# Kernel tuning notes

Measured on AMD Instinct MI355X. Metric: run time of the kernel, lower is better.

## Reference

```python
import jax, jax.numpy as jnp
import numpy as np

N_HEADS = 16
HID_DIM = 64
INPUT_DIM = 1024
B, L = 4, 1024
NEG = -10000000000.0


def setup_inputs() -> dict:
    key = jax.random.key(0)
    ks = jax.random.split(key, 10)
    d = INPUT_DIM
    h = N_HEADS * HID_DIM
    s = 1.0 / np.sqrt(d)
    return {
        "query": jax.random.normal(ks[0], (B, L, d), dtype=jnp.float32),
        "key": jax.random.normal(ks[1], (B, L, d), dtype=jnp.float32),
        "value": jax.random.normal(ks[2], (B, L, d), dtype=jnp.float32),
        "mask": jax.random.randint(ks[3], (B, 1, L, L), 0, 2, dtype=jnp.int32),
        "wq": jax.random.normal(ks[4], (d, h), dtype=jnp.float32) * s,
        "bq": jnp.zeros((h,), dtype=jnp.float32),
        "wk": jax.random.normal(ks[5], (d, h), dtype=jnp.float32) * s,
        "bk": jnp.zeros((h,), dtype=jnp.float32),
        "wv": jax.random.normal(ks[6], (d, h), dtype=jnp.float32) * s,
        "bv": jnp.zeros((h,), dtype=jnp.float32),
    }


def _split_heads(x):
    # [B, L, H*D] -> [B, H, L, D]
    b, l, _ = x.shape
    return x.reshape(b, l, N_HEADS, HID_DIM).transpose(0, 2, 1, 3)


def reference(query, key, value, mask, wq, bq, wk, bk, wv, bv):
    scale = jnp.sqrt(jnp.float32(HID_DIM))
    Q = _split_heads(query @ wq + bq)   # [B,H,L,D]
    K = _split_heads(key @ wk + bk)
    V = _split_heads(value @ wv + bv)
    energy = jnp.einsum("bhqd,bhkd->bhqk", Q, K) / scale
    energy = jnp.where(mask == 0, jnp.float32(NEG), energy)
    attention = energy  # NOTE: softmax is intentionally skipped, as in the source
    x = jnp.einsum("bhqk,bhkd->bhqd", attention, V)
    x = x.transpose(0, 2, 1, 3).reshape(query.shape[0], -1, N_HEADS * HID_DIM)
    return (attention, x)
```

## Files before the change

### kernel.cpp

```cpp
#include <hip/hip_runtime.h>
#include <stdint.h>
#include <stddef.h>


typedef __attribute__((ext_vector_type(8))) short short8;
typedef __attribute__((ext_vector_type(4))) float f32x4;
typedef __attribute__((ext_vector_type(4))) int i32x4;
typedef __attribute__((ext_vector_type(2))) unsigned int u32x2;

#define MFMA16(a, b, c) __builtin_amdgcn_mfma_f32_16x16x32_bf16(a, b, c, 0, 0, 0)

using gptr_t = const __attribute__((address_space(1))) void*;
using lptr_t = __attribute__((address_space(3))) void*;

#define NEGV -10000000000.0f

__device__ __forceinline__ unsigned short f2bf(float f) {
  uint32_t u = __builtin_bit_cast(uint32_t, f);
  u += 0x7FFFu + ((u >> 16) & 1u);
  return (unsigned short)(u >> 16);
}

__global__ __launch_bounds__(256) void k_maskpack(const int* __restrict__ mask,
                                                  unsigned long long* __restrict__ mb) {
  const int wid = (blockIdx.x * 256 + threadIdx.x) >> 6;
  const int l = threadIdx.x & 63;
#pragma unroll 4
  for (int i = 0; i < 32; ++i) {
    const size_t c = (size_t)wid * 32 + i;
    const int v = mask[c * 64 + l];
    const unsigned long long bits = __ballot(v != 0);
    if (l == 0) mb[c] = bits;
  }
}

__global__ __launch_bounds__(256) void k_wt(
    const float* __restrict__ wq, const float* __restrict__ wk, const float* __restrict__ wv,
    unsigned short* __restrict__ tq, unsigned short* __restrict__ tk,
    unsigned short* __restrict__ tv) {
  const int z = blockIdx.z;
  const float* src = z == 0 ? wq : z == 1 ? wk : wv;
  unsigned short* dst = z == 0 ? tq : z == 1 ? tk : tv;
  __shared__ unsigned short t[64][65];
  const int n0 = blockIdx.x * 64, k0 = blockIdx.y * 64;
#pragma unroll
  for (int i = 0; i < 16; ++i) {
    const int idx = i * 256 + threadIdx.x;
    const int r = idx >> 6, c = idx & 63;
    t[r][c] = f2bf(src[(size_t)(k0 + r) * 1024 + n0 + c]);
  }
  __syncthreads();
#pragma unroll
  for (int i = 0; i < 16; ++i) {
    const int idx = i * 256 + threadIdx.x;
    const int r = idx >> 6, c = idx & 63;
    dst[(size_t)(n0 + r) * 1024 + k0 + c] = t[c][r];
  }
}

__global__ __launch_bounds__(256) void k_gemm(
    const float* __restrict__ Xq, const float* __restrict__ Xk,
    const float* __restrict__ Xv,
    const unsigned short* __restrict__ Wq, const unsigned short* __restrict__ Wk,
    const unsigned short* __restrict__ Wv,
    const float* __restrict__ bq, const float* __restrict__ bk, const float* __restrict__ bv,
    unsigned short* __restrict__ Cq, unsigned short* __restrict__ Ck,
    unsigned short* __restrict__ Vt) {
  const int z = blockIdx.z;
  const float* X           = z == 0 ? Xq : z == 1 ? Xk : Xv;
  const unsigned short* Wt = z == 0 ? Wq : z == 1 ? Wk : Wv;
  const float* bias        = z == 0 ? bq : z == 1 ? bk : bv;

  __shared__ unsigned short Ads[128 * 64];
  __shared__ unsigned short Bds[128 * 64];

  const int tid = threadIdx.x;
  const int w = tid >> 6, l = tid & 63;
  const int lr = l & 15, g = l >> 4;
  const int m0 = blockIdx.y * 128, n0 = blockIdx.x * 128;
  const int wm = (w >> 1) * 64, wn = (w & 1) * 64;
  const int srow = tid >> 3, sslot = tid & 7;

  f32x4 acc[4][4];
#pragma unroll
  for (int mi = 0; mi < 4; ++mi)
#pragma unroll
    for (int ni = 0; ni < 4; ++ni) acc[mi][ni] = (f32x4){0.f, 0.f, 0.f, 0.f};

  for (int kt = 0; kt < 16; ++kt) {
    const int kb = kt * 64;
#pragma unroll
    for (int i = 0; i < 4; ++i) {
      const int idx = i * 256 + tid;
      const int row = idx >> 3, c8 = idx & 7;
      const float* ga = X + (size_t)(m0 + row) * 1024 + kb + c8 * 8;
      f32x4 a0 = *(const f32x4*)ga;
      f32x4 a1 = *(const f32x4*)(ga + 4);
      short8 pk;
      pk[0] = (short)f2bf(a0[0]); pk[1] = (short)f2bf(a0[1]);
      pk[2] = (short)f2bf(a0[2]); pk[3] = (short)f2bf(a0[3]);
      pk[4] = (short)f2bf(a1[0]); pk[5] = (short)f2bf(a1[1]);
      pk[6] = (short)f2bf(a1[2]); pk[7] = (short)f2bf(a1[3]);
      *(short8*)&Ads[row * 64 + ((c8 ^ (row & 7)) << 3)] = pk;
    }
#pragma unroll
    for (int i = 0; i < 4; ++i) {
      const int row = i * 32 + srow;
      const int scol = ((sslot ^ (row & 7)) << 3);
      const unsigned short* gb = Wt + (size_t)(n0 + row) * 1024 + kb + scol;
      __builtin_amdgcn_global_load_lds((gptr_t)gb, (lptr_t)&Bds[(i * 32 + w * 8) * 64], 16, 0, 0);
    }
    __syncthreads();
    short8 afr[4][2], bfr[4][2];
#pragma unroll
    for (int t = 0; t < 4; ++t)
#pragma unroll
      for (int ks = 0; ks < 2; ++ks) {
        const int ra = wm + t * 16 + lr;
        afr[t][ks] = *(const short8*)&Ads[ra * 64 + (((ks * 4 + g) ^ (ra & 7)) << 3)];
        const int rb = wn + t * 16 + lr;
        bfr[t][ks] = *(const short8*)&Bds[rb * 64 + (((ks * 4 + g) ^ (rb & 7)) << 3)];
      }
#pragma unroll
    for (int ks = 0; ks < 2; ++ks)
#pragma unroll
      for (int mi = 0; mi < 4; ++mi)
#pragma unroll
        for (int ni = 0; ni < 4; ++ni)
          acc[mi][ni] = MFMA16(afr[mi][ks], bfr[ni][ks], acc[mi][ni]);
    __syncthreads();
  }

  if (z != 2) {
    unsigned short* C = z == 0 ? Cq : Ck;
#pragma unroll
    for (int mi = 0; mi < 4; ++mi)
#pragma unroll
      for (int ni = 0; ni < 4; ++ni) {
        const int n = n0 + wn + ni * 16 + lr;
        const float bs = bias[n];
        f32x4 a = acc[mi][ni];
#pragma unroll
        for (int r = 0; r < 4; ++r) {
          const int m = m0 + wm + mi * 16 + g * 4 + r;
          C[(size_t)m * 1024 + n] = f2bf(a[r] + bs);
        }
      }
  } else {
#pragma unroll
    for (int mi = 0; mi < 4; ++mi)
#pragma unroll
      for (int ni = 0; ni < 4; ++ni) {
        const int ng = n0 + wn + ni * 16 + lr;
        const int hh = ng >> 6, dd = ng & 63;
        const float bs = bias[ng];
        f32x4 a = acc[mi][ni];
        const int mg = m0 + wm + mi * 16 + g * 4;
        const int bb = mg >> 10;
        const int ll = mg & 1023;
        u32x2 pk;
        pk[0] = (uint32_t)f2bf(a[0] + bs) | ((uint32_t)f2bf(a[1] + bs) << 16);
        pk[1] = (uint32_t)f2bf(a[2] + bs) | ((uint32_t)f2bf(a[3] + bs) << 16);
        *(u32x2*)&Vt[(size_t)((bb * 16 + hh) * 64 + dd) * 1024 + ll] = pk;
      }
  }
}

__global__ __launch_bounds__(512, 4) void k_attn(
    const unsigned short* __restrict__ Qb, const unsigned short* __restrict__ Kb,
    const unsigned short* __restrict__ Vt, const uint32_t* __restrict__ mb,
    float* __restrict__ att, float* __restrict__ xout) {
  const int bh = blockIdx.y, b = bh >> 4, h = bh & 15;
  const int tid = threadIdx.x;
  const int w = tid >> 6, l = tid & 63;
  const int lr = l & 15, g = l >> 4;
  const int q0 = blockIdx.x * 128 + w * 16;

  __shared__ unsigned short Kl[128 * 64];
  __shared__ unsigned short Vl[64 * 128];
  __shared__ unsigned short Pl[8 * 16 * 128];
  unsigned short* Pw = &Pl[w * 16 * 128];

  short8 qf[2];
#pragma unroll
  for (int ks = 0; ks < 2; ++ks)
    qf[ks] = *(const short8*)&Qb[(size_t)(b * 1024 + q0 + lr) * 1024 +
                                 h * 64 + ks * 32 + g * 8];

  f32x4 xacc[4];
#pragma unroll
  for (int di = 0; di < 4; ++di) xacc[di] = (f32x4){0.f, 0.f, 0.f, 0.f};

  for (int kt = 0; kt < 8; ++kt) {
    const int kb = kt * 128;
    __syncthreads();
#pragma unroll
    for (int i = 0; i < 2; ++i) {
      const int row = i * 64 + (tid >> 3);
      const int slot = tid & 7;
      const unsigned short* src = Kb + (size_t)(b * 1024 + kb + row) * 1024 +
                                  h * 64 + ((slot ^ (row & 7)) << 3);
      __builtin_amdgcn_global_load_lds((gptr_t)src, (lptr_t)&Kl[(i * 64 + w * 8) * 64], 16, 0, 0);
    }
#pragma unroll
    for (int i = 0; i < 2; ++i) {
      const int row = i * 32 + (tid >> 4);
      const int slot = tid & 15;
      const unsigned short* src = Vt + (size_t)(bh * 64 + row) * 1024 + kb +
                                  ((slot ^ (row & 7)) << 3);
      __builtin_amdgcn_global_load_lds((gptr_t)src, (lptr_t)&Vl[(i * 32 + w * 4) * 128], 16, 0, 0);
    }
    const i32x4 mw = *(const i32x4*)&mb[(size_t)(b * 1024 + q0 + lr) * 32 + kt * 4];
    __syncthreads();

    f32x4 s[8];
#pragma unroll
    for (int ni = 0; ni < 8; ++ni) {
      f32x4 a = (f32x4){0.f, 0.f, 0.f, 0.f};
#pragma unroll
      for (int ks = 0; ks < 2; ++ks) {
        const int row = ni * 16 + lr;
        short8 kf = *(const short8*)&Kl[row * 64 + (((ks * 4 + g) ^ (row & 7)) << 3)];
        a = MFMA16(kf, qf[ks], a);
      }
      s[ni] = a;
    }
#pragma unroll
    for (int ni = 0; ni < 8; ++ni) {
      const uint32_t wbits = (uint32_t)mw[ni >> 1];
      const int bit0 = (ni & 1) * 16 + g * 4;
      f32x4 e;
#pragma unroll
      for (int j = 0; j < 4; ++j)
        e[j] = ((wbits >> (bit0 + j)) & 1u) ? s[ni][j] * 0.125f : NEGV;
      u32x2 pk;
      pk[0] = (uint32_t)f2bf(e[0]) | ((uint32_t)f2bf(e[1]) << 16);
      pk[1] = (uint32_t)f2bf(e[2]) | ((uint32_t)f2bf(e[3]) << 16);
      const int colq = ni * 16 + g * 4;
      *(u32x2*)&Pw[lr * 128 + (colq ^ ((lr & 7) << 3))] = pk;
    }
    asm volatile("s_waitcnt lgkmcnt(0)" ::: "memory");
    __builtin_amdgcn_sched_barrier(0);
#pragma unroll
    for (int p = 0; p < 8; ++p) {
      const int flat = p * 256 + l * 4;
      const int row = flat >> 7;
      const int col = flat & 127;
      u32x2 pr = *(const u32x2*)&Pw[row * 128 + (col ^ ((row & 7) << 3))];
      const uint32_t u0 = pr[0], u1 = pr[1];
      f32x4 e;
      e[0] = __builtin_bit_cast(float, u0 << 16);
      e[1] = __builtin_bit_cast(float, u0 & 0xFFFF0000u);
      e[2] = __builtin_bit_cast(float, u1 << 16);
      e[3] = __builtin_bit_cast(float, u1 & 0xFFFF0000u);
      __builtin_nontemporal_store(
          e, (f32x4*)&att[(size_t)(bh * 1024 + q0 + row) * 1024 + kb + col]);
    }
#pragma unroll
    for (int ks4 = 0; ks4 < 4; ++ks4) {
      const int colk = ks4 * 32 + g * 8;
      short8 pa = *(const short8*)&Pw[lr * 128 + (colk ^ ((lr & 7) << 3))];
#pragma unroll
      for (int di = 0; di < 4; ++di) {
        const int vr = di * 16 + lr;
        short8 vf = *(const short8*)&Vl[vr * 128 + (colk ^ ((vr & 7) << 3))];
        xacc[di] = MFMA16(pa, vf, xacc[di]);
      }
    }
    asm volatile("" ::: "memory");
  }

#pragma unroll
  for (int di = 0; di < 4; ++di) {
    f32x4 a = xacc[di];
#pragma unroll
    for (int r = 0; r < 4; ++r) {
      const int q = q0 + g * 4 + r;
      __builtin_nontemporal_store(
          a[r], &xout[(size_t)(b * 1024 + q) * 1024 + h * 64 + di * 16 + lr]);
    }
  }
}

extern "C" void kernel_launch(void* const* d_in, const int* in_sizes, int n_in,
                              void* d_out, int out_size, void* d_ws, size_t ws_size,
                              hipStream_t stream) {
  (void)in_sizes; (void)n_in; (void)out_size;
  const float* q   = (const float*)d_in[0];
  const float* k   = (const float*)d_in[1];
  const float* v   = (const float*)d_in[2];
  const int* mask  = (const int*)d_in[3];
  const float* wq  = (const float*)d_in[4];
  const float* bq  = (const float*)d_in[5];
  const float* wk  = (const float*)d_in[6];
  const float* bk  = (const float*)d_in[7];
  const float* wv  = (const float*)d_in[8];
  const float* bv  = (const float*)d_in[9];
  float* att = (float*)d_out;
  float* x   = att + (size_t)4 * 16 * 1024 * 1024;

  char* ws = (char*)d_ws;
  const size_t SZX = (size_t)4096 * 1024 * 2;
  const size_t SZW = (size_t)1024 * 1024 * 2;
  const size_t SZM = (size_t)4 * 1024 * 32 * 4;
  if (ws_size < 3 * SZX + 3 * SZW + SZM) return;
  unsigned short* Wtq = (unsigned short*)(ws);
  unsigned short* Wtk = (unsigned short*)(ws + SZW);
  unsigned short* Wtv = (unsigned short*)(ws + 2 * SZW);
  unsigned short* Qb  = (unsigned short*)(ws + 3 * SZW);
  unsigned short* Kb  = (unsigned short*)(ws + 3 * SZW + SZX);
  unsigned short* Vt  = (unsigned short*)(ws + 3 * SZW + 2 * SZX);
  unsigned long long* Mb = (unsigned long long*)(ws + 3 * SZW + 3 * SZX);

  k_maskpack<<<dim3(512), 256, 0, stream>>>(mask, Mb);
  k_wt<<<dim3(16, 16, 3), 256, 0, stream>>>(wq, wk, wv, Wtq, Wtk, Wtv);
  k_gemm<<<dim3(8, 32, 3), 256, 0, stream>>>(q, k, v, Wtq, Wtk, Wtv,
                                             bq, bk, bv, Qb, Kb, Vt);
  k_attn<<<dim3(8, 64), 512, 0, stream>>>(Qb, Kb, Vt, (const uint32_t*)Mb,
                                          att, x);
}
```

Before: 175.1 us.

## Double-buffer K/V tiles in LDS and process P in half-width chunks

K and V tiles now use two LDS buffers. The next tile's global-to-LDS loads and mask word are issued before computing on the current tile, so only one barrier per iteration remains, guarded by a partial vmcnt wait. The bf16 P staging buffer is halved: each 128-column tile is written, read back for the attention store and fed to the PV MFMAs in two 64-column halves with a new swizzle. This aims to hide K/V load latency behind compute, at the cost of more LDS per block and a vmcnt count that depends on the exact store and load issue order.

Result: no change. 174.5 us (-0.4%).

```diff
diff --git a/kernel.cpp b/kernel.cpp
--- a/kernel.cpp
+++ b/kernel.cpp
@@ -176,10 +176,31 @@
   const int lr = l & 15, g = l >> 4;
   const int q0 = blockIdx.x * 128 + w * 16;
 
-  __shared__ unsigned short Kl[128 * 64];
-  __shared__ unsigned short Vl[64 * 128];
-  __shared__ unsigned short Pl[8 * 16 * 128];
-  unsigned short* Pw = &Pl[w * 16 * 128];
+  __shared__ unsigned short Kl[2][128 * 64];
+  __shared__ unsigned short Vl[2][64 * 128];
+  __shared__ unsigned short Pl[8][16 * 64];
+  unsigned short* Pw = Pl[w];
+
+#define STAGE_KV(t, bb)                                                          \
+  do {                                                                           \
+    const int kbs = (t) * 128;                                                   \
+    _Pragma("unroll") for (int i = 0; i < 2; ++i) {                              \
+      const int row = i * 64 + (tid >> 3);                                       \
+      const int slot = tid & 7;                                                  \
+      const unsigned short* src = Kb + (size_t)(b * 1024 + kbs + row) * 1024 +   \
+                                  h * 64 + ((slot ^ (row & 7)) << 3);            \
+      __builtin_amdgcn_global_load_lds((gptr_t)src,                              \
+          (lptr_t)&Kl[bb][(i * 64 + w * 8) * 64], 16, 0, 0);                     \
+    }                                                                            \
+    _Pragma("unroll") for (int i = 0; i < 2; ++i) {                              \
+      const int row = i * 32 + (tid >> 4);                                       \
+      const int slot = tid & 15;                                                 \
+      const unsigned short* src = Vt + (size_t)(bh * 64 + row) * 1024 + kbs +    \
+                                  ((slot ^ (row & 7)) << 3);                     \
+      __builtin_amdgcn_global_load_lds((gptr_t)src,                              \
+          (lptr_t)&Vl[bb][(i * 32 + w * 4) * 128], 16, 0, 0);                    \
+    }                                                                            \
+  } while (0)
 
   short8 qf[2];
 #pragma unroll
@@ -191,27 +212,20 @@
 #pragma unroll
   for (int di = 0; di < 4; ++di) xacc[di] = (f32x4){0.f, 0.f, 0.f, 0.f};
 
+  const size_t mrow = (size_t)(b * 1024 + q0 + lr) * 32;
+
+  STAGE_KV(0, 0);
+  i32x4 mwc = *(const i32x4*)&mb[mrow];
+  asm volatile("s_waitcnt vmcnt(0)" ::: "memory");
+  __builtin_amdgcn_s_barrier();
+  __builtin_amdgcn_sched_barrier(0);
+
   for (int kt = 0; kt < 8; ++kt) {
+    const int cur = kt & 1;
     const int kb = kt * 128;
-    __syncthreads();
-#pragma unroll
-    for (int i = 0; i < 2; ++i) {
-      const int row = i * 64 + (tid >> 3);
-      const int slot = tid & 7;
-      const unsigned short* src = Kb + (size_t)(b * 1024 + kb + row) * 1024 +
-                                  h * 64 + ((slot ^ (row & 7)) << 3);
-      __builtin_amdgcn_global_load_lds((gptr_t)src, (lptr_t)&Kl[(i * 64 + w * 8) * 64], 16, 0, 0);
-    }
-#pragma unroll
-    for (int i = 0; i < 2; ++i) {
-      const int row = i * 32 + (tid >> 4);
-      const int slot = tid & 15;
-      const unsigned short* src = Vt + (size_t)(bh * 64 + row) * 1024 + kb +
-                                  ((slot ^ (row & 7)) << 3);
-      __builtin_amdgcn_global_load_lds((gptr_t)src, (lptr_t)&Vl[(i * 32 + w * 4) * 128], 16, 0, 0);
-    }
-    const i32x4 mw = *(const i32x4*)&mb[(size_t)(b * 1024 + q0 + lr) * 32 + kt * 4];
-    __syncthreads();
+    if (kt < 7) STAGE_KV(kt + 1, cur ^ 1);
+    i32x4 mwn = mwc;
+    if (kt < 7) mwn = *(const i32x4*)&mb[mrow + (kt + 1) * 4];
 
     f32x4 s[8];
 #pragma unroll
@@ -220,55 +234,69 @@
 #pragma unroll
       for (int ks = 0; ks < 2; ++ks) {
         const int row = ni * 16 + lr;
-        short8 kf = *(const short8*)&Kl[row * 64 + (((ks * 4 + g) ^ (row & 7)) << 3)];
+        short8 kf = *(const short8*)&Kl[cur][row * 64 + (((ks * 4 + g) ^ (row & 7)) << 3)];
         a = MFMA16(kf, qf[ks], a);
       }
       s[ni] = a;
     }
-#pragma unroll
-    for (int ni = 0; ni < 8; ++ni) {
-      const uint32_t wbits = (uint32_t)mw[ni >> 1];
-      const int bit0 = (ni & 1) * 16 + g * 4;
-      f32x4 e;
-#pragma unroll
-      for (int j = 0; j < 4; ++j)
-        e[j] = ((wbits >> (bit0 + j)) & 1u) ? s[ni][j] * 0.125f : NEGV;
-      u32x2 pk;
-      pk[0] = (uint32_t)f2bf(e[0]) | ((uint32_t)f2bf(e[1]) << 16);
-      pk[1] = (uint32_t)f2bf(e[2]) | ((uint32_t)f2bf(e[3]) << 16);
-      const int colq = ni * 16 + g * 4;
-      *(u32x2*)&Pw[lr * 128 + (colq ^ ((lr & 7) << 3))] = pk;
-    }
-    asm volatile("s_waitcnt lgkmcnt(0)" ::: "memory");
-    __builtin_amdgcn_sched_barrier(0);
-#pragma unroll
-    for (int p = 0; p < 8; ++p) {
-      const int flat = p * 256 + l * 4;
-      const int row = flat >> 7;
-      const int col = flat & 127;
-      u32x2 pr = *(const u32x2*)&Pw[row * 128 + (col ^ ((row & 7) << 3))];
-      const uint32_t u0 = pr[0], u1 = pr[1];
-      f32x4 e;
-      e[0] = __builtin_bit_cast(float, u0 << 16);
-      e[1] = __builtin_bit_cast(float, u0 & 0xFFFF0000u);
-      e[2] = __builtin_bit_cast(float, u1 << 16);
-      e[3] = __builtin_bit_cast(float, u1 & 0xFFFF0000u);
-      __builtin_nontemporal_store(
-          e, (f32x4*)&att[(size_t)(bh * 1024 + q0 + row) * 1024 + kb + col]);
-    }
-#pragma unroll
-    for (int ks4 = 0; ks4 < 4; ++ks4) {
-      const int colk = ks4 * 32 + g * 8;
-      short8 pa = *(const short8*)&Pw[lr * 128 + (colk ^ ((lr & 7) << 3))];
-#pragma unroll
-      for (int di = 0; di < 4; ++di) {
-        const int vr = di * 16 + lr;
-        short8 vf = *(const short8*)&Vl[vr * 128 + (colk ^ ((vr & 7) << 3))];
-        xacc[di] = MFMA16(pa, vf, xacc[di]);
-      }
-    }
-    asm volatile("" ::: "memory");
-  }
+
+#pragma unroll
+    for (int hh = 0; hh < 2; ++hh) {
+#pragma unroll
+      for (int n2 = 0; n2 < 4; ++n2) {
+        const int ni = hh * 4 + n2;
+        const uint32_t wbits = (uint32_t)mwc[ni >> 1];
+        const int bit0 = (ni & 1) * 16 + g * 4;
+        f32x4 e;
+#pragma unroll
+        for (int j = 0; j < 4; ++j)
+          e[j] = ((wbits >> (bit0 + j)) & 1u) ? s[ni][j] * 0.125f : NEGV;
+        u32x2 pk;
+        pk[0] = (uint32_t)f2bf(e[0]) | ((uint32_t)f2bf(e[1]) << 16);
+        pk[1] = (uint32_t)f2bf(e[2]) | ((uint32_t)f2bf(e[3]) << 16);
+        const int c16 = n2 * 2 + (g >> 1);
+        *(u32x2*)&Pw[lr * 64 + ((c16 ^ (lr & 7)) << 3) + (g & 1) * 4] = pk;
+      }
+      asm volatile("s_waitcnt lgkmcnt(0)" ::: "memory");
+      __builtin_amdgcn_sched_barrier(0);
+#pragma unroll
+      for (int p = 0; p < 4; ++p) {
+        const int row = p * 4 + g;
+        const int c16 = lr >> 1;
+        u32x2 pr = *(const u32x2*)&Pw[row * 64 + ((c16 ^ (row & 7)) << 3) + (lr & 1) * 4];
+        const uint32_t u0 = pr[0], u1 = pr[1];
+        f32x4 e;
+        e[0] = __builtin_bit_cast(float, u0 << 16);
+        e[1] = __builtin_bit_cast(float, u0 & 0xFFFF0000u);
+        e[2] = __builtin_bit_cast(float, u1 << 16);
+        e[3] = __builtin_bit_cast(float, u1 & 0xFFFF0000u);
+        __builtin_nontemporal_store(
+            e, (f32x4*)&att[(size_t)(bh * 1024 + q0 + row) * 1024 + kb + hh * 64 + lr * 4]);
+      }
+#pragma unroll
+      for (int k2 = 0; k2 < 2; ++k2) {
+        const int c16 = k2 * 4 + g;
+        short8 pa = *(const short8*)&Pw[lr * 64 + ((c16 ^ (lr & 7)) << 3)];
+        const int colk = hh * 64 + k2 * 32 + g * 8;
+#pragma unroll
+        for (int di = 0; di < 4; ++di) {
+          const int vr = di * 16 + lr;
+          short8 vf = *(const short8*)&Vl[cur][vr * 128 + (colk ^ ((vr & 7) << 3))];
+          xacc[di] = MFMA16(pa, vf, xacc[di]);
+        }
+      }
+      asm volatile("s_waitcnt lgkmcnt(0)" ::: "memory");
+      __builtin_amdgcn_sched_barrier(0);
+    }
+
+    mwc = mwn;
+    if (kt < 7) {
+      asm volatile("s_waitcnt vmcnt(9)" ::: "memory");
+      __builtin_amdgcn_s_barrier();
+      __builtin_amdgcn_sched_barrier(0);
+    }
+  }
+#undef STAGE_KV
 
 #pragma unroll
   for (int di = 0; di < 4; ++di) {
```
